# Optimization experiments

Measured on AMD Instinct MI355X. Metric: run time of the kernel, lower is better.

Reference implementation:

```python
import jax, jax.numpy as jnp
import numpy as np

L, D, H, P = 4096, 512, 512, 16  # seq_len, feature_dim, attention_hidden_dim, padding_size


def setup_inputs() -> dict:
    key = jax.random.key(0)
    k1, k2, k3, k4 = jax.random.split(key, 4)
    x = jax.random.normal(k1, (L, D), dtype=jnp.float32)
    s = 1.0 / np.sqrt(D).astype(np.float32)
    Ww = jax.random.uniform(k2, (H, D), jnp.float32, -s, s)   # nn.Linear(D, H, bias=False).weight
    Wu = jax.random.uniform(k3, (H, D), jnp.float32, -s, s)
    sv = 1.0 / np.sqrt(H).astype(np.float32)
    Wv = jax.random.uniform(k4, (1, H), jnp.float32, -sv, sv)  # nn.Linear(H, 1, bias=False).weight
    return {"x": x, "Ww": Ww, "Wu": Wu, "Wv": Wv}


def _window_gather(x):
    # zero-pad P rows on each end of the sequence, then for each position i
    # gather the 2P neighbors (P left, P right), excluding the center.
    xp = jnp.pad(x, ((P, P), (0, 0)))
    off = jnp.concatenate([jnp.arange(P), jnp.arange(P + 1, 2 * P + 1)])  # [2P]
    idx = jnp.arange(x.shape[0])[:, None] + off[None, :]                  # [L, 2P]
    return xp[idx]                                                        # [L, 2P, D]


def reference(x, Ww, Wu, Wv):
    x_local = _window_gather(x)                                  # [L, 2P, D]
    wx = x @ Ww.T                                                # [L, H] (center, computed once vs torch repeat)
    ux = jnp.einsum('lwd,hd->lwh', x_local, Wu)                  # [L, 2P, H]
    energy = jnp.tanh(wx[:, None, :] + ux)                       # [L, 2P, H]
    scores = jnp.einsum('lwh,h->lw', energy, Wv[0])              # [L, 2P]
    attn = jax.nn.softmax(scores, axis=1)                        # softmax over window
    g = jnp.einsum('lw,lwd->ld', attn, x_local)                  # [L, D]
    return g
```

## Files before the change

kernel.cpp:

```cpp
#include <hip/hip_runtime.h>

#define L_SEQ 4096
#define D_DIM 512
#define H_DIM 512
#define P_PAD 16
#define LB 4
#define NR (LB + 2 * P_PAD)
#define LOG2E2 2.885390081777927f
#define LOG2E  1.4426950408889634f

typedef __bf16 bf16x8 __attribute__((ext_vector_type(8)));
typedef float  f32x4  __attribute__((ext_vector_type(4)));
typedef unsigned short u16x8 __attribute__((ext_vector_type(8)));

extern "C" __device__ float __ocml_native_exp2_f32(float);

__device__ __forceinline__ float exp2_fast(float x) {
#if __has_builtin(__builtin_amdgcn_exp2f)
    return __builtin_amdgcn_exp2f(x);
#else
    return __ocml_native_exp2_f32(x);
#endif
}

__device__ __forceinline__ ushort f2bf(float f) {
    unsigned u = __float_as_uint(f);
    return (ushort)((u + 0x7FFFu + ((u >> 16) & 1u)) >> 16);
}
__device__ __forceinline__ float bf2f(ushort s) {
    return __uint_as_float((unsigned)s << 16);
}

__device__ __forceinline__ float readlane_f(float v, int sl) {
    return __uint_as_float(__builtin_amdgcn_readlane(__float_as_uint(v), sl));
}

__global__ __launch_bounds__(256) void convert_kernel(
    const float* __restrict__ x, const float* __restrict__ Ww,
    const float* __restrict__ Wu, ushort* __restrict__ xb,
    ushort* __restrict__ Wwb, ushort* __restrict__ Wub)
{
    int i = blockIdx.x * 256 + threadIdx.x;
    const float* src; ushort* dst; int off;
    if (i < 524288)      { src = x;  dst = xb;  off = i; }
    else if (i < 589824) { src = Ww; dst = Wwb; off = i - 524288; }
    else                 { src = Wu; dst = Wub; off = i - 589824; }
    float4 v = ((const float4*)src)[off];
    ushort4 o;
    o.x = f2bf(v.x); o.y = f2bf(v.y); o.z = f2bf(v.z); o.w = f2bf(v.w);
    ((ushort4*)dst)[off] = o;
}

__global__ __launch_bounds__(256, 2) void dual_gemm_mfma(
    const ushort* __restrict__ xb, const ushort* __restrict__ Wwb,
    const ushort* __restrict__ Wub, ushort* __restrict__ Ewb, ushort* __restrict__ Eub)
{
    const ushort* Bm = blockIdx.z ? Wub : Wwb;
    ushort*      out = blockIdx.z ? Eub : Ewb;
    const int m0 = blockIdx.x * 128;
    const int n0 = blockIdx.y * 64;

    __shared__ __align__(16) ushort As[2][128 * 64];
    __shared__ __align__(16) ushort Bs[2][64 * 64];

    const int tid  = threadIdx.x;
    const int wv   = tid >> 6;
    const int lane = tid & 63;
    const int wm   = (wv >> 1) * 64;
    const int wn   = (wv & 1) * 32;
    const int lr   = lane & 15;
    const int lg   = lane >> 4;
    const int rx   = lr & 7;

    f32x4 acc[4][2] = {};

    auto stage = [&](int t, int buf) {
        const int k0 = t * 64;
        #pragma unroll
        for (int i = 0; i < 4; ++i) {
            int c = i * 256 + tid;
            int row = c >> 3, q = c & 7;
            const ushort* src = xb + (size_t)(m0 + row) * D_DIM + k0 + ((q ^ (row & 7)) * 8);
            ushort* dst = &As[buf][(i * 256 + wv * 64) * 8];
            __builtin_amdgcn_global_load_lds(
                (const __attribute__((address_space(1))) void*)src,
                (__attribute__((address_space(3))) void*)dst, 16, 0, 0);
        }
        #pragma unroll
        for (int i = 0; i < 2; ++i) {
            int c = i * 256 + tid;
            int row = c >> 3, q = c & 7;
            const ushort* src = Bm + (size_t)(n0 + row) * D_DIM + k0 + ((q ^ (row & 7)) * 8);
            ushort* dst = &Bs[buf][(i * 256 + wv * 64) * 8];
            __builtin_amdgcn_global_load_lds(
                (const __attribute__((address_space(1))) void*)src,
                (__attribute__((address_space(3))) void*)dst, 16, 0, 0);
        }
    };

    auto compute = [&](int buf) {
        #pragma unroll
        for (int kk = 0; kk < 2; ++kk) {
            bf16x8 a[4], b[2];
            #pragma unroll
            for (int mi = 0; mi < 4; ++mi)
                a[mi] = *(const bf16x8*)&As[buf][(wm + mi * 16 + lr) * 64 +
                                                 (((kk * 4 + lg) ^ rx) * 8)];
            #pragma unroll
            for (int ni = 0; ni < 2; ++ni)
                b[ni] = *(const bf16x8*)&Bs[buf][(wn + ni * 16 + lr) * 64 +
                                                 (((kk * 4 + lg) ^ rx) * 8)];
            #pragma unroll
            for (int mi = 0; mi < 4; ++mi)
                #pragma unroll
                for (int ni = 0; ni < 2; ++ni)
                    acc[mi][ni] = __builtin_amdgcn_mfma_f32_16x16x32_bf16(
                        a[mi], b[ni], acc[mi][ni], 0, 0, 0);
        }
    };

    stage(0, 0);
    __syncthreads();
    #pragma unroll
    for (int t = 0; t < 7; ++t) {
        stage(t + 1, (t + 1) & 1);
        compute(t & 1);
        __syncthreads();
    }
    compute(1);

    #pragma unroll
    for (int mi = 0; mi < 4; ++mi)
        #pragma unroll
        for (int ni = 0; ni < 2; ++ni)
            #pragma unroll
            for (int r = 0; r < 4; ++r)
                out[(size_t)(m0 + wm + mi * 16 + lg * 4 + r) * H_DIM + n0 + wn + ni * 16 + lr] =
                    f2bf(exp2_fast(LOG2E2 * acc[mi][ni][r]));
}

__global__ __launch_bounds__(512, 2) void scores_kernel(
    const ushort* __restrict__ Ewb, const ushort* __restrict__ Eub,
    const float* __restrict__ Wv, float* __restrict__ attn)
{
    const int l    = (blockIdx.x & 7) * 512 + (blockIdx.x >> 3);
    const int wg   = threadIdx.x >> 6;
    const int lane = threadIdx.x & 63;

    __shared__ float sc_lds[32];

    float ewr[8], wvn[8];
    {
        u16x8 ew8 = *(const u16x8*)&Ewb[(size_t)l * H_DIM + lane * 8];
        const f32x4* wvp = (const f32x4*)&Wv[lane * 8];
        f32x4 v0 = wvp[0], v1 = wvp[1];
        #pragma unroll
        for (int e = 0; e < 8; ++e) ewr[e] = bf2f(ew8[e]);
        #pragma unroll
        for (int e = 0; e < 4; ++e) { wvn[e] = -2.0f * v0[e]; wvn[e + 4] = -2.0f * v1[e]; }
    }

    float aoob = 0.0f;
    if (l < P_PAD || l >= L_SEQ - P_PAD) {
        #pragma unroll
        for (int e = 0; e < 8; ++e)
            aoob = __builtin_fmaf(wvn[e], __builtin_amdgcn_rcpf(ewr[e] + 1.0f), aoob);
    }

    u16x8 u[4];
    int valid[4];
    #pragma unroll
    for (int wi = 0; wi < 4; ++wi) {
        const int w = wg * 4 + wi;
        const int j = (w < P_PAD) ? (w - P_PAD) : (w - P_PAD + 1);
        int n = l + j;
        valid[wi] = ((unsigned)n < (unsigned)L_SEQ);
        n = min(max(n, 0), L_SEQ - 1);
        u[wi] = *(const u16x8*)&Eub[(size_t)n * H_DIM + lane * 8];
    }
    float a4[4];
    #pragma unroll
    for (int wi = 0; wi < 4; ++wi) {
        float a = 0.0f;
        #pragma unroll
        for (int e = 0; e < 8; ++e) {
            float eu = bf2f(u[wi][e]);
            float q  = __builtin_fmaf(ewr[e], eu, 1.0f);
            a = __builtin_fmaf(wvn[e], __builtin_amdgcn_rcpf(q), a);
        }
        a4[wi] = valid[wi] ? a : aoob;
    }

    const bool b0 = lane & 1, b1 = lane & 2;
    float s01 = b0 ? a4[0] : a4[1];
    float r01 = __shfl_xor(s01, 1);
    float c0  = (b0 ? a4[1] : a4[0]) + r01;
    float s23 = b0 ? a4[2] : a4[3];
    float r23 = __shfl_xor(s23, 1);
    float c1  = (b0 ? a4[3] : a4[2]) + r23;
    float s2  = b1 ? c0 : c1;
    float r2  = __shfl_xor(s2, 2);
    float c   = (b1 ? c1 : c0) + r2;
    c += __shfl_xor(c, 4);
    c += __shfl_xor(c, 8);
    c += __shfl_xor(c, 16);
    c += __shfl_xor(c, 32);
    if (lane < 4) sc_lds[wg * 4 + lane] = c;
    __syncthreads();

    if (threadIdx.x < 32) {
        float s0 = sc_lds[threadIdx.x];
        float m = s0;
        #pragma unroll
        for (int off = 16; off; off >>= 1) m = fmaxf(m, __shfl_xor(m, off, 32));
        float e = exp2_fast((s0 - m) * LOG2E);
        float sum = e;
        #pragma unroll
        for (int off = 16; off; off >>= 1) sum += __shfl_xor(sum, off, 32);
        attn[l * 32 + threadIdx.x] = e * __builtin_amdgcn_rcpf(sum);
    }
}

template<bool EDGE>
__device__ __forceinline__ void gather_body(
    const float* __restrict__ x, const float* __restrict__ attn,
    float* __restrict__ g, int l0, int tid)
{
    const int d    = tid * 2;
    const int lane = tid & 63;

    float2 aw2 = *(const float2*)&attn[l0 * 32 + lane * 2];

    float2 xv[NR];
    #pragma unroll
    for (int t = 0; t < NR; ++t) {
        int n = l0 - P_PAD + t;
        if (EDGE) n = min(max(n, 0), L_SEQ - 1);
        xv[t] = *(const float2*)&x[(size_t)n * D_DIM + d];
    }

    #pragma unroll
    for (int li = 0; li < LB; ++li) {
        float ax = 0.0f, ay = 0.0f;
        #pragma unroll
        for (int w = 0; w < 32; ++w) {
            const int j = (w < P_PAD) ? (w - P_PAD) : (w - P_PAD + 1);
            const int t = j + P_PAD + li;
            const int k = li * 32 + w;
            float aw = readlane_f((k & 1) ? aw2.y : aw2.x, k >> 1);
            if (EDGE) {
                const int n = l0 + li + j;
                if (n < 0 || n >= L_SEQ) aw = 0.0f;
            }
            ax = __builtin_fmaf(aw, xv[t].x, ax);
            ay = __builtin_fmaf(aw, xv[t].y, ay);
        }
        *(float2*)&g[(size_t)(l0 + li) * D_DIM + d] = make_float2(ax, ay);
    }
}

__global__ __launch_bounds__(256, 4) void gather_kernel(
    const float* __restrict__ x, const float* __restrict__ attn,
    float* __restrict__ g)
{
    const int bid = (blockIdx.x & 7) * 128 + (blockIdx.x >> 3);
    const int l0  = bid * LB;
    const int tid = threadIdx.x;

    if (l0 >= P_PAD && l0 + LB + P_PAD <= L_SEQ)
        gather_body<false>(x, attn, g, l0, tid);
    else
        gather_body<true>(x, attn, g, l0, tid);
}

extern "C" void kernel_launch(void* const* d_in, const int* in_sizes, int n_in,
                              void* d_out, int out_size, void* d_ws, size_t ws_size,
                              hipStream_t stream) {
    const float* x  = (const float*)d_in[0];
    const float* Ww = (const float*)d_in[1];
    const float* Wu = (const float*)d_in[2];
    const float* Wv = (const float*)d_in[3];
    float* g = (float*)d_out;

    ushort* Ewb = (ushort*)d_ws;
    ushort* Eub = Ewb + (size_t)L_SEQ * H_DIM;
    ushort* xb  = Eub + (size_t)L_SEQ * H_DIM;
    ushort* Wwb = xb + (size_t)L_SEQ * D_DIM;
    ushort* Wub = Wwb + (size_t)H_DIM * D_DIM;
    float* attn = (float*)(Wub + (size_t)H_DIM * D_DIM);

    convert_kernel<<<dim3(2560), 256, 0, stream>>>(x, Ww, Wu, xb, Wwb, Wub);
    dual_gemm_mfma<<<dim3(L_SEQ / 128, H_DIM / 64, 2), 256, 0, stream>>>(xb, Wwb, Wub, Ewb, Eub);
    scores_kernel<<<dim3(L_SEQ), 512, 0, stream>>>(Ewb, Eub, Wv, attn);
    gather_kernel<<<dim3(L_SEQ / LB), 256, 0, stream>>>(x, attn, g);
}
```

Before: 43.14 us.

## Fuse bf16 conversion into GEMM staging and merge scores with gather

Removes the separate fp32-to-bf16 conversion kernel: the GEMM now loads fp32 x and weights directly, converts them in registers, and writes swizzled bf16 into LDS. This replaces the async global-to-LDS loads with synchronous register-staged loads. The scores and gather kernels are merged into one kernel that handles 4 rows per block with 512 threads. Attention weights stay in LDS instead of going through global memory. This drops two launches and the intermediate buffers, but reads of fp32 x are duplicated across the N-tiles of the GEMM and the staging loads can no longer overlap with compute.

```diff
diff --git a/kernel.cpp b/kernel.cpp
--- a/kernel.cpp
+++ b/kernel.cpp
@@ -35,27 +35,11 @@
     return __uint_as_float(__builtin_amdgcn_readlane(__float_as_uint(v), sl));
 }
 
-__global__ __launch_bounds__(256) void convert_kernel(
+__global__ __launch_bounds__(256, 2) void dual_gemm_mfma(
     const float* __restrict__ x, const float* __restrict__ Ww,
-    const float* __restrict__ Wu, ushort* __restrict__ xb,
-    ushort* __restrict__ Wwb, ushort* __restrict__ Wub)
+    const float* __restrict__ Wu, ushort* __restrict__ Ewb, ushort* __restrict__ Eub)
 {
-    int i = blockIdx.x * 256 + threadIdx.x;
-    const float* src; ushort* dst; int off;
-    if (i < 524288)      { src = x;  dst = xb;  off = i; }
-    else if (i < 589824) { src = Ww; dst = Wwb; off = i - 524288; }
-    else                 { src = Wu; dst = Wub; off = i - 589824; }
-    float4 v = ((const float4*)src)[off];
-    ushort4 o;
-    o.x = f2bf(v.x); o.y = f2bf(v.y); o.z = f2bf(v.z); o.w = f2bf(v.w);
-    ((ushort4*)dst)[off] = o;
-}
-
-__global__ __launch_bounds__(256, 2) void dual_gemm_mfma(
-    const ushort* __restrict__ xb, const ushort* __restrict__ Wwb,
-    const ushort* __restrict__ Wub, ushort* __restrict__ Ewb, ushort* __restrict__ Eub)
-{
-    const ushort* Bm = blockIdx.z ? Wub : Wwb;
+    const float* Bw = blockIdx.z ? Wu : Ww;
     ushort*      out = blockIdx.z ? Eub : Ewb;
     const int m0 = blockIdx.x * 128;
     const int n0 = blockIdx.y * 64;
@@ -78,23 +62,25 @@
         const int k0 = t * 64;
         #pragma unroll
         for (int i = 0; i < 4; ++i) {
-            int c = i * 256 + tid;
-            int row = c >> 3, q = c & 7;
-            const ushort* src = xb + (size_t)(m0 + row) * D_DIM + k0 + ((q ^ (row & 7)) * 8);
-            ushort* dst = &As[buf][(i * 256 + wv * 64) * 8];
-            __builtin_amdgcn_global_load_lds(
-                (const __attribute__((address_space(1))) void*)src,
-                (__attribute__((address_space(3))) void*)dst, 16, 0, 0);
+            int c = i * 256 + tid, row = c >> 3, q = c & 7;
+            const float* s = x + (size_t)(m0 + row) * D_DIM + k0 + q * 8;
+            float4 f0 = *(const float4*)s;
+            float4 f1 = *(const float4*)(s + 4);
+            u16x8 hv;
+            hv[0] = f2bf(f0.x); hv[1] = f2bf(f0.y); hv[2] = f2bf(f0.z); hv[3] = f2bf(f0.w);
+            hv[4] = f2bf(f1.x); hv[5] = f2bf(f1.y); hv[6] = f2bf(f1.z); hv[7] = f2bf(f1.w);
+            *(u16x8*)&As[buf][row * 64 + ((q ^ (row & 7)) * 8)] = hv;
         }
         #pragma unroll
         for (int i = 0; i < 2; ++i) {
-            int c = i * 256 + tid;
-            int row = c >> 3, q = c & 7;
-            const ushort* src = Bm + (size_t)(n0 + row) * D_DIM + k0 + ((q ^ (row & 7)) * 8);
-            ushort* dst = &Bs[buf][(i * 256 + wv * 64) * 8];
-            __builtin_amdgcn_global_load_lds(
-                (const __attribute__((address_space(1))) void*)src,
-                (__attribute__((address_space(3))) void*)dst, 16, 0, 0);
+            int c = i * 256 + tid, row = c >> 3, q = c & 7;
+            const float* s = Bw + (size_t)(n0 + row) * D_DIM + k0 + q * 8;
+            float4 f0 = *(const float4*)s;
+            float4 f1 = *(const float4*)(s + 4);
+            u16x8 hv;
+            hv[0] = f2bf(f0.x); hv[1] = f2bf(f0.y); hv[2] = f2bf(f0.z); hv[3] = f2bf(f0.w);
+            hv[4] = f2bf(f1.x); hv[5] = f2bf(f1.y); hv[6] = f2bf(f1.z); hv[7] = f2bf(f1.w);
+            *(u16x8*)&Bs[buf][row * 64 + ((q ^ (row & 7)) * 8)] = hv;
         }
     };
 
@@ -139,15 +125,19 @@
                     f2bf(exp2_fast(LOG2E2 * acc[mi][ni][r]));
 }
 
-__global__ __launch_bounds__(512, 2) void scores_kernel(
+template<bool EDGE>
+__device__ __forceinline__ void fused_body(
     const ushort* __restrict__ Ewb, const ushort* __restrict__ Eub,
-    const float* __restrict__ Wv, float* __restrict__ attn)
+    const float* __restrict__ Wv, const float* __restrict__ x,
+    float* __restrict__ g, int l0,
+    float sc_lds[LB][32], float at_lds[LB][32])
 {
-    const int l    = (blockIdx.x & 7) * 512 + (blockIdx.x >> 3);
-    const int wg   = threadIdx.x >> 6;
-    const int lane = threadIdx.x & 63;
-
-    __shared__ float sc_lds[32];
+    const int tid  = threadIdx.x;
+    const int wv   = tid >> 6;
+    const int lane = tid & 63;
+    const int li   = wv >> 1;
+    const int half = wv & 1;
+    const int l    = l0 + li;
 
     float ewr[8], wvn[8];
     {
@@ -161,55 +151,64 @@
     }
 
     float aoob = 0.0f;
-    if (l < P_PAD || l >= L_SEQ - P_PAD) {
+    if (EDGE && (l < P_PAD || l >= L_SEQ - P_PAD)) {
         #pragma unroll
         for (int e = 0; e < 8; ++e)
             aoob = __builtin_fmaf(wvn[e], __builtin_amdgcn_rcpf(ewr[e] + 1.0f), aoob);
     }
 
-    u16x8 u[4];
-    int valid[4];
-    #pragma unroll
-    for (int wi = 0; wi < 4; ++wi) {
-        const int w = wg * 4 + wi;
-        const int j = (w < P_PAD) ? (w - P_PAD) : (w - P_PAD + 1);
-        int n = l + j;
-        valid[wi] = ((unsigned)n < (unsigned)L_SEQ);
-        n = min(max(n, 0), L_SEQ - 1);
-        u[wi] = *(const u16x8*)&Eub[(size_t)n * H_DIM + lane * 8];
-    }
-    float a4[4];
-    #pragma unroll
-    for (int wi = 0; wi < 4; ++wi) {
-        float a = 0.0f;
-        #pragma unroll
-        for (int e = 0; e < 8; ++e) {
-            float eu = bf2f(u[wi][e]);
-            float q  = __builtin_fmaf(ewr[e], eu, 1.0f);
-            a = __builtin_fmaf(wvn[e], __builtin_amdgcn_rcpf(q), a);
-        }
-        a4[wi] = valid[wi] ? a : aoob;
-    }
-
-    const bool b0 = lane & 1, b1 = lane & 2;
-    float s01 = b0 ? a4[0] : a4[1];
-    float r01 = __shfl_xor(s01, 1);
-    float c0  = (b0 ? a4[1] : a4[0]) + r01;
-    float s23 = b0 ? a4[2] : a4[3];
-    float r23 = __shfl_xor(s23, 1);
-    float c1  = (b0 ? a4[3] : a4[2]) + r23;
-    float s2  = b1 ? c0 : c1;
-    float r2  = __shfl_xor(s2, 2);
-    float c   = (b1 ? c1 : c0) + r2;
-    c += __shfl_xor(c, 4);
-    c += __shfl_xor(c, 8);
-    c += __shfl_xor(c, 16);
-    c += __shfl_xor(c, 32);
-    if (lane < 4) sc_lds[wg * 4 + lane] = c;
+    const ushort* base = Eub + (size_t)l * H_DIM + lane * 8;
+    #pragma unroll
+    for (int q = 0; q < 4; ++q) {
+        u16x8 u[4];
+        int valid[4];
+        #pragma unroll
+        for (int wi = 0; wi < 4; ++wi) {
+            const int w = half * 16 + q * 4 + wi;
+            const int j = (w < P_PAD) ? (w - P_PAD) : (w - P_PAD + 1);
+            if (EDGE) {
+                int n = l + j;
+                valid[wi] = ((unsigned)n < (unsigned)L_SEQ);
+                n = min(max(n, 0), L_SEQ - 1);
+                u[wi] = *(const u16x8*)&Eub[(size_t)n * H_DIM + lane * 8];
+            } else {
+                u[wi] = *(const u16x8*)(base + j * H_DIM);
+            }
+        }
+        float a4[4];
+        #pragma unroll
+        for (int wi = 0; wi < 4; ++wi) {
+            float a = 0.0f;
+            #pragma unroll
+            for (int e = 0; e < 8; ++e) {
+                float eu = bf2f(u[wi][e]);
+                float qq = __builtin_fmaf(ewr[e], eu, 1.0f);
+                a = __builtin_fmaf(wvn[e], __builtin_amdgcn_rcpf(qq), a);
+            }
+            if (EDGE) a = valid[wi] ? a : aoob;
+            a4[wi] = a;
+        }
+        const bool b0 = lane & 1, b1 = lane & 2;
+        float s01 = b0 ? a4[0] : a4[1];
+        float r01 = __shfl_xor(s01, 1);
+        float c0  = (b0 ? a4[1] : a4[0]) + r01;
+        float s23 = b0 ? a4[2] : a4[3];
+        float r23 = __shfl_xor(s23, 1);
+        float c1  = (b0 ? a4[3] : a4[2]) + r23;
+        float s2  = b1 ? c0 : c1;
+        float r2  = __shfl_xor(s2, 2);
+        float c   = (b1 ? c1 : c0) + r2;
+        c += __shfl_xor(c, 4);
+        c += __shfl_xor(c, 8);
+        c += __shfl_xor(c, 16);
+        c += __shfl_xor(c, 32);
+        if (lane < 4) sc_lds[li][half * 16 + q * 4 + lane] = c;
+    }
     __syncthreads();
 
-    if (threadIdx.x < 32) {
-        float s0 = sc_lds[threadIdx.x];
+    if (tid < LB * 32) {
+        const int ll = tid >> 5, w = tid & 31;
+        float s0 = sc_lds[ll][w];
         float m = s0;
         #pragma unroll
         for (int off = 16; off; off >>= 1) m = fmaxf(m, __shfl_xor(m, off, 32));
@@ -217,60 +216,55 @@
         float sum = e;
         #pragma unroll
         for (int off = 16; off; off >>= 1) sum += __shfl_xor(sum, off, 32);
-        attn[l * 32 + threadIdx.x] = e * __builtin_amdgcn_rcpf(sum);
-    }
-}
-
-template<bool EDGE>
-__device__ __forceinline__ void gather_body(
-    const float* __restrict__ x, const float* __restrict__ attn,
-    float* __restrict__ g, int l0, int tid)
-{
-    const int d    = tid * 2;
-    const int lane = tid & 63;
-
-    float2 aw2 = *(const float2*)&attn[l0 * 32 + lane * 2];
-
-    float2 xv[NR];
+        at_lds[ll][w] = e * __builtin_amdgcn_rcpf(sum);
+    }
+    __syncthreads();
+
+    const int col = tid;
+    float2 aw2 = ((const float2*)at_lds)[lane];
+
+    float xv[NR];
     #pragma unroll
     for (int t = 0; t < NR; ++t) {
         int n = l0 - P_PAD + t;
         if (EDGE) n = min(max(n, 0), L_SEQ - 1);
-        xv[t] = *(const float2*)&x[(size_t)n * D_DIM + d];
-    }
-
-    #pragma unroll
-    for (int li = 0; li < LB; ++li) {
-        float ax = 0.0f, ay = 0.0f;
+        xv[t] = x[(size_t)n * D_DIM + col];
+    }
+
+    #pragma unroll
+    for (int li2 = 0; li2 < LB; ++li2) {
+        float a = 0.0f;
         #pragma unroll
         for (int w = 0; w < 32; ++w) {
             const int j = (w < P_PAD) ? (w - P_PAD) : (w - P_PAD + 1);
-            const int t = j + P_PAD + li;
-            const int k = li * 32 + w;
+            const int t = j + P_PAD + li2;
+            const int k = li2 * 32 + w;
             float aw = readlane_f((k & 1) ? aw2.y : aw2.x, k >> 1);
             if (EDGE) {
-                const int n = l0 + li + j;
+                const int n = l0 + li2 + j;
                 if (n < 0 || n >= L_SEQ) aw = 0.0f;
             }
-            ax = __builtin_fmaf(aw, xv[t].x, ax);
-            ay = __builtin_fmaf(aw, xv[t].y, ay);
-        }
-        *(float2*)&g[(size_t)(l0 + li) * D_DIM + d] = make_float2(ax, ay);
-    }
-}
-
-__global__ __launch_bounds__(256, 4) void gather_kernel(
-    const float* __restrict__ x, const float* __restrict__ attn,
+            a = __builtin_fmaf(aw, xv[t], a);
+        }
+        g[(size_t)(l0 + li2) * D_DIM + col] = a;
+    }
+}
+
+__global__ __launch_bounds__(512, 4) void scores_gather_kernel(
+    const ushort* __restrict__ Ewb, const ushort* __restrict__ Eub,
+    const float* __restrict__ Wv, const float* __restrict__ x,
     float* __restrict__ g)
 {
     const int bid = (blockIdx.x & 7) * 128 + (blockIdx.x >> 3);
     const int l0  = bid * LB;
-    const int tid = threadIdx.x;
+
+    __shared__ __align__(16) float sc_lds[LB][32];
+    __shared__ __align__(16) float at_lds[LB][32];
 
     if (l0 >= P_PAD && l0 + LB + P_PAD <= L_SEQ)
-        gather_body<false>(x, attn, g, l0, tid);
+        fused_body<false>(Ewb, Eub, Wv, x, g, l0, sc_lds, at_lds);
     else
-        gather_body<true>(x, attn, g, l0, tid);
+        fused_body<true>(Ewb, Eub, Wv, x, g, l0, sc_lds, at_lds);
 }
 
 extern "C" void kernel_launch(void* const* d_in, const int* in_sizes, int n_in,
@@ -284,13 +278,7 @@
 
     ushort* Ewb = (ushort*)d_ws;
     ushort* Eub = Ewb + (size_t)L_SEQ * H_DIM;
-    ushort* xb  = Eub + (size_t)L_SEQ * H_DIM;
-    ushort* Wwb = xb + (size_t)L_SEQ * D_DIM;
-    ushort* Wub = Wwb + (size_t)H_DIM * D_DIM;
-    float* attn = (float*)(Wub + (size_t)H_DIM * D_DIM);
-
-    convert_kernel<<<dim3(2560), 256, 0, stream>>>(x, Ww, Wu, xb, Wwb, Wub);
-    dual_gemm_mfma<<<dim3(L_SEQ / 128, H_DIM / 64, 2), 256, 0, stream>>>(xb, Wwb, Wub, Ewb, Eub);
-    scores_kernel<<<dim3(L_SEQ), 512, 0, stream>>>(Ewb, Eub, Wv, attn);
-    gather_kernel<<<dim3(L_SEQ / LB), 256, 0, stream>>>(x, attn, g);
-}
+
+    dual_gemm_mfma<<<dim3(L_SEQ / 128, H_DIM / 64, 2), 256, 0, stream>>>(x, Ww, Wu, Ewb, Eub);
+    scores_gather_kernel<<<dim3(L_SEQ / LB), 512, 0, stream>>>(Ewb, Eub, Wv, x, g);
+}
```

New measurement: 37.81 us. 1.14x faster.
